# Kernel tuning notes

Hardware: AMD Instinct MI355X
Metric: run time of the kernel (lower is better)

## Reference

```python
import jax, jax.numpy as jnp
import numpy as np

E = 8   # number of experts (= laac_size)
A = 8   # number of agents
B = 2048
S = 256   # per-agent input feature size
H1, H2 = 512, 256          # shallow_dims
D0, D1, D2 = 256, 512, 128  # deep_dims


def setup_inputs() -> dict:
    key = jax.random.key(0)
    ks = jax.random.split(key, 11)
    inputs = jax.random.normal(ks[0], (A, B, S), dtype=jnp.float32)
    laac_shallow = jax.random.randint(ks[1], (1, A), 0, E, dtype=jnp.int64)
    laac_deep = jax.random.randint(ks[2], (1, A), 0, E, dtype=jnp.int64)
    def w(k, shape, fan_in):
        return jax.random.normal(k, shape, dtype=jnp.float32) / np.sqrt(fan_in)
    return {
        "inputs": inputs,
        "laac_shallow": laac_shallow,
        "laac_deep": laac_deep,
        "Ws1": w(ks[3], (E, S, H1), S),  "bs1": jnp.zeros((E, H1), jnp.float32),
        "Ws2": w(ks[4], (E, H1, H2), H1), "bs2": jnp.zeros((E, H2), jnp.float32),
        "Wd1": w(ks[5], (E, D0, D1), D0), "bd1": jnp.zeros((E, D1), jnp.float32),
        "Wd2": w(ks[6], (E, D1, D2), D1), "bd2": jnp.zeros((E, D2), jnp.float32),
    }


def reference(inputs, laac_shallow, laac_deep, Ws1, bs1, Ws2, bs2, Wd1, bd1, Wd2, bd2):
    agent_ids = jnp.arange(A)
    # --- shallow experts: every expert applied to full stacked input [A,B,S] ---
    # Linear -> ReLU -> Linear -> ReLU (final_activation)
    h = jax.nn.relu(jnp.einsum('abi,eih->eabh', inputs, Ws1) + bs1[:, None, None, :])  # [E,A,B,H1]
    sh = jax.nn.relu(jnp.einsum('eabh,eho->eabo', h, Ws2) + bs2[:, None, None, :])     # [E,A,B,H2]
    sel_s = laac_shallow.T[:, 0]             # [A] expert id per agent
    deep_in = sh[sel_s, agent_ids]           # gather over expert dim -> [A,B,H2]
    # --- deep experts: Linear -> ReLU -> Linear (no final activation) ---
    d = jax.nn.relu(jnp.einsum('abi,eih->eabh', deep_in, Wd1) + bd1[:, None, None, :])  # [E,A,B,D1]
    dout = jnp.einsum('eabh,eho->eabo', d, Wd2) + bd2[:, None, None, :]                 # [E,A,B,D2]
    sel_d = laac_deep.T[:, 0]
    out = dout[sel_d, agent_ids]             # [A,B,D2] (original returns this split per agent)
    return out
```

## Files before the change

### kernel.cpp

```cpp
#include <hip/hip_runtime.h>
#include <hip/hip_bf16.h>


typedef __attribute__((ext_vector_type(8))) short bf16x8;
typedef __attribute__((ext_vector_type(4))) float f32x4;

__device__ __forceinline__ ushort f2b(float x) {
    __hip_bfloat16 h = __float2bfloat16(x);
    return *reinterpret_cast<ushort*>(&h);
}

__global__ __launch_bounds__(256)
void prep_weights(const float* __restrict__ Ws1, const float* __restrict__ Ws2,
                  const float* __restrict__ Wd1, const float* __restrict__ Wd2,
                  const int* __restrict__ sel_s, const int* __restrict__ sel_d,
                  ushort* __restrict__ W1p, ushort* __restrict__ W2p,
                  ushort* __restrict__ W3p, ushort* __restrict__ W4p)
{
    const int layer = blockIdx.z;
    const int e  = blockIdx.y;
    const int fg = blockIdx.x;

    const int* sel = (layer <= 1) ? sel_s : sel_d;
    bool used = false;
    #pragma unroll
    for (int a = 0; a < 8; ++a) used |= (sel[a] == e);
    if (!used) return;

    const float* W; ushort* Wp; int K, N;
    if (layer == 0)      { W = Ws1; Wp = W1p; K = 256; N = 512; }
    else if (layer == 1) { W = Ws2; Wp = W2p; K = 512; N = 256; }
    else if (layer == 2) { W = Wd1; Wp = W3p; K = 256; N = 512; }
    else                 { W = Wd2; Wp = W4p; K = 512; N = 128; }
    if (fg >= N / 16) return;
    const int NK = K / 32;
    W += (size_t)e * K * N;

    __shared__ float tile[512][17];
    const int tid = threadIdx.x;
    const int n0 = fg * 16;
    for (int idx = tid; idx < K * 16; idx += 256)
        tile[idx >> 4][idx & 15] = W[(size_t)(idx >> 4) * N + n0 + (idx & 15)];
    __syncthreads();
    ushort* dst = Wp + (((size_t)e * (N / 16) + fg) * NK) * 512;
    for (int w = tid; w < NK * 64; w += 256) {
        const int s    = w >> 6;
        const int lane = w & 63;
        const int c    = lane & 15;
        const int kb   = s * 32 + ((lane >> 4) << 3);
        bf16x8 v;
        #pragma unroll
        for (int j = 0; j < 8; ++j)
            v[j] = (short)f2b(tile[kb + j][c]);
        *reinterpret_cast<bf16x8*>(&dst[(size_t)w * 8]) = v;
    }
}

template<int K, int N, int MG>
__device__ __forceinline__ bf16x8 peekB(const ushort* __restrict__ Wp,
                                        int wid, int lane, int j)
{
    constexpr int NG = 16 / MG;
    constexpr int F  = N / 16 / NG;
    constexpr int NK = K / 32;
    const int wc = wid % NG;
    const ushort* bBase = Wp + ((size_t)(wc * F) * NK) * 512 + (size_t)lane * 8;
    const int f = j % F, s = j / F;
    return *reinterpret_cast<const bf16x8*>(bBase + ((size_t)f * NK + s) * 512);
}

__device__ __forceinline__ bf16x8 peekB4(const ushort* __restrict__ Wp,
                                         int wid, int lane, int j)
{
    const int wc = wid & 7;
    const int kh = wid >> 3;
    return *reinterpret_cast<const bf16x8*>(
        Wp + ((size_t)wc * 16 + kh * 8 + j) * 512 + (size_t)lane * 8);
}

template<int K, int N, int MG, int RELU>
__device__ __forceinline__ void layer_mlp(
    const ushort* __restrict__ Wp, const float* __restrict__ bias,
    const ushort* __restrict__ sIn, ushort* __restrict__ sOut,
    float* __restrict__ gOut, int wid, int lane,
    bf16x8 pb0, bf16x8 pb1)
{
    constexpr int NG = 16 / MG;
    constexpr int F  = N / 16 / NG;
    constexpr int M4 = 4 / MG;
    constexpr int NK = K / 32;
    const int r15 = lane & 15, lh = lane >> 4;
    const int wc = wid % NG, wr = wid / NG;
    const int rowBase = wr * (64 / MG);

    const ushort* bBase = Wp + ((size_t)(wc * F) * NK) * 512 + (size_t)lane * 8;

    float4 bv[F];
    #pragma unroll
    for (int f = 0; f < F; ++f)
        bv[f] = *reinterpret_cast<const float4*>(
            &bias[(wc * F + f) * 16 + lh * 4]);

    f32x4 acc[M4][F];
    #pragma unroll
    for (int m = 0; m < M4; ++m)
        #pragma unroll
        for (int f = 0; f < F; ++f)
            acc[m][f] = (f32x4){0.f, 0.f, 0.f, 0.f};

    #pragma unroll
    for (int s = 0; s < NK; ++s) {
        const int k0 = s * 32;
        bf16x8 a[M4];
        #pragma unroll
        for (int m = 0; m < M4; ++m) {
            const int row  = rowBase + m * 16 + r15;
            const int phys = ((k0 >> 3) + lh) ^ (row & 7);
            a[m] = *reinterpret_cast<const bf16x8*>(
                reinterpret_cast<const char*>(sIn) + row * (K * 2) + (phys << 4));
        }
        bf16x8 b[F];
        #pragma unroll
        for (int f = 0; f < F; ++f) {
            const int j = s * F + f;
            if (j == 0)      b[f] = pb0;
            else if (j == 1) b[f] = pb1;
            else b[f] = *reinterpret_cast<const bf16x8*>(
                     bBase + ((size_t)f * NK + s) * 512);
        }
        #pragma unroll
        for (int m = 0; m < M4; ++m)
            #pragma unroll
            for (int f = 0; f < F; ++f)
                acc[m][f] = __builtin_amdgcn_mfma_f32_16x16x32_bf16(
                    b[f], a[m], acc[m][f], 0, 0, 0);
    }

    #pragma unroll
    for (int f = 0; f < F; ++f) {
        const int cbase = (wc * F + f) * 16 + lh * 4;
        #pragma unroll
        for (int m = 0; m < M4; ++m) {
            const int row = rowBase + m * 16 + r15;
            float v0 = acc[m][f][0] + bv[f].x;
            float v1 = acc[m][f][1] + bv[f].y;
            float v2 = acc[m][f][2] + bv[f].z;
            float v3 = acc[m][f][3] + bv[f].w;
            if (RELU) {
                v0 = fmaxf(v0, 0.f); v1 = fmaxf(v1, 0.f);
                v2 = fmaxf(v2, 0.f); v3 = fmaxf(v3, 0.f);
            }
            if (gOut) {
                *reinterpret_cast<float4*>(&gOut[(size_t)row * N + cbase]) =
                    (float4){v0, v1, v2, v3};
            } else {
                const uint lo = ((uint)f2b(v1) << 16) | (uint)f2b(v0);
                const uint hi = ((uint)f2b(v3) << 16) | (uint)f2b(v2);
                const int byteoff = row * (N * 2) +
                    ((((cbase >> 3) ^ (row & 7))) << 4) + ((cbase & 7) << 1);
                *reinterpret_cast<uint2*>(
                    reinterpret_cast<char*>(sOut) + byteoff) = (uint2){lo, hi};
            }
        }
    }
}

__device__ __forceinline__ int pidx(int row, int col) {
    const int chunk = col >> 2;
    const int phys  = chunk ^ ((row & 7) << 2);
    return row * 128 + (phys << 2);
}

__device__ __forceinline__ void layer_out_ksplit(
    const ushort* __restrict__ Wp, const float* __restrict__ bias,
    const ushort* __restrict__ sIn, float* __restrict__ pLds,
    float* __restrict__ gOut, int wid, int lane,
    bf16x8 pb0, bf16x8 pb1)
{
    constexpr int K = 512, N = 128;
    constexpr int NKH = 8;
    const int r15 = lane & 15, lh = lane >> 4;
    const int wc = wid & 7;
    const int kh = wid >> 3;

    const ushort* bBase = Wp + ((size_t)wc * 16 + kh * 8) * 512 + (size_t)lane * 8;

    const float4 bv = *reinterpret_cast<const float4*>(&bias[wc * 16 + lh * 4]);

    f32x4 acc[4];
    #pragma unroll
    for (int m = 0; m < 4; ++m) acc[m] = (f32x4){0.f, 0.f, 0.f, 0.f};

    #pragma unroll
    for (int s2 = 0; s2 < NKH; ++s2) {
        const int k0 = (kh * NKH + s2) * 32;
        bf16x8 a[4];
        #pragma unroll
        for (int m = 0; m < 4; ++m) {
            const int row  = m * 16 + r15;
            const int phys = ((k0 >> 3) + lh) ^ (row & 7);
            a[m] = *reinterpret_cast<const bf16x8*>(
                reinterpret_cast<const char*>(sIn) + row * (K * 2) + (phys << 4));
        }
        bf16x8 b;
        if (s2 == 0)      b = pb0;
        else if (s2 == 1) b = pb1;
        else b = *reinterpret_cast<const bf16x8*>(bBase + (size_t)s2 * 512);
        #pragma unroll
        for (int m = 0; m < 4; ++m)
            acc[m] = __builtin_amdgcn_mfma_f32_16x16x32_bf16(
                b, a[m], acc[m], 0, 0, 0);
    }

    if (kh == 1) {
        #pragma unroll
        for (int m = 0; m < 4; ++m) {
            const int row = m * 16 + r15;
            const int col = wc * 16 + lh * 4;
            *reinterpret_cast<float4*>(&pLds[pidx(row, col)]) =
                (float4){acc[m][0], acc[m][1], acc[m][2], acc[m][3]};
        }
    }
    __syncthreads();
    if (kh == 0) {
        #pragma unroll
        for (int m = 0; m < 4; ++m) {
            const int row = m * 16 + r15;
            const int col = wc * 16 + lh * 4;
            const float4 p = *reinterpret_cast<const float4*>(&pLds[pidx(row, col)]);
            const float v0 = acc[m][0] + p.x + bv.x;
            const float v1 = acc[m][1] + p.y + bv.y;
            const float v2 = acc[m][2] + p.z + bv.z;
            const float v3 = acc[m][3] + p.w + bv.w;
            *reinterpret_cast<float4*>(&gOut[(size_t)row * N + col]) =
                (float4){v0, v1, v2, v3};
        }
    }
}

__global__ __launch_bounds__(1024, 4)
void madps_fused(const float* __restrict__ X,
                 const int* __restrict__ sel_s, const int* __restrict__ sel_d,
                 const ushort* __restrict__ W1p, const ushort* __restrict__ W2p,
                 const ushort* __restrict__ W3p, const ushort* __restrict__ W4p,
                 const float* __restrict__ bs1, const float* __restrict__ bs2,
                 const float* __restrict__ bd1, const float* __restrict__ bd2,
                 float* __restrict__ out)
{
    constexpr int S = 256, H1 = 512, H2 = 256, D1 = 512, D2 = 128;

    __shared__ __align__(16) ushort buf0[64 * 256];
    __shared__ __align__(16) ushort buf1[64 * 512];

    const int bid   = blockIdx.x;
    const int agent = bid & 7;
    const int rb    = bid >> 3;
    const int tid   = threadIdx.x;
    const int lane  = tid & 63;
    const int wid   = tid >> 6;

    const long long es = sel_s[agent];
    const long long ed = sel_d[agent];

    const ushort* W1e = W1p + (size_t)es * ((H1 / 16) * (S  / 32) * 512);
    const ushort* W2e = W2p + (size_t)es * ((H2 / 16) * (H1 / 32) * 512);
    const ushort* W3e = W3p + (size_t)ed * ((D1 / 16) * (H2 / 32) * 512);
    const ushort* W4e = W4p + (size_t)ed * ((D2 / 16) * (D1 / 32) * 512);

    const float* Xa = X + ((size_t)agent * 2048 + (size_t)rb * 64) * S;

    bf16x8 pb0 = peekB<S, H1, 1>(W1e, wid, lane, 0);
    bf16x8 pb1 = peekB<S, H1, 1>(W1e, wid, lane, 1);

    #pragma unroll
    for (int i = 0; i < 4; ++i) {
        const int flat4 = i * 1024 + tid;
        const int row = flat4 >> 6;
        const int c4  = flat4 & 63;
        const float4 v = reinterpret_cast<const float4*>(Xa)[flat4];
        ushort4 o;
        o.x = f2b(v.x); o.y = f2b(v.y); o.z = f2b(v.z); o.w = f2b(v.w);
        const int byteoff = (((c4 >> 1) ^ (row & 7)) << 4) | ((c4 & 1) << 3);
        *reinterpret_cast<ushort4*>(
            reinterpret_cast<char*>(buf0) + row * 512 + byteoff) = o;
    }
    __syncthreads();

    layer_mlp<S, H1, 1, 1>(W1e, bs1 + es * H1, buf0, buf1, nullptr,
                           wid, lane, pb0, pb1);
    pb0 = peekB<H1, H2, 1>(W2e, wid, lane, 0);
    pb1 = peekB<H1, H2, 1>(W2e, wid, lane, 1);
    __syncthreads();
    layer_mlp<H1, H2, 1, 1>(W2e, bs2 + es * H2, buf1, buf0, nullptr,
                            wid, lane, pb0, pb1);
    pb0 = peekB<H2, D1, 1>(W3e, wid, lane, 0);
    pb1 = peekB<H2, D1, 1>(W3e, wid, lane, 1);
    __syncthreads();
    layer_mlp<H2, D1, 1, 1>(W3e, bd1 + ed * D1, buf0, buf1, nullptr,
                            wid, lane, pb0, pb1);
    pb0 = peekB4(W4e, wid, lane, 0);
    pb1 = peekB4(W4e, wid, lane, 1);
    __syncthreads();
    float* outP = out + ((size_t)agent * 2048 + (size_t)rb * 64) * D2;
    layer_out_ksplit(W4e, bd2 + ed * D2, buf1,
                     reinterpret_cast<float*>(buf0), outP, wid, lane, pb0, pb1);
}

extern "C" void kernel_launch(void* const* d_in, const int* in_sizes, int n_in,
                              void* d_out, int out_size, void* d_ws, size_t ws_size,
                              hipStream_t stream)
{
    constexpr int E = 8, S = 256, H1 = 512, H2 = 256, D1 = 512, D2 = 128;

    const float* inputs = (const float*)d_in[0];
    const int*   sel_s  = (const int*)d_in[1];
    const int*   sel_d  = (const int*)d_in[2];
    const float* Ws1 = (const float*)d_in[3];
    const float* bs1 = (const float*)d_in[4];
    const float* Ws2 = (const float*)d_in[5];
    const float* bs2 = (const float*)d_in[6];
    const float* Wd1 = (const float*)d_in[7];
    const float* bd1 = (const float*)d_in[8];
    const float* Wd2 = (const float*)d_in[9];
    const float* bd2 = (const float*)d_in[10];
    float* out = (float*)d_out;

    ushort* W1p = (ushort*)d_ws;
    ushort* W2p = W1p + (size_t)E * S * H1;
    ushort* W3p = W2p + (size_t)E * H1 * H2;
    ushort* W4p = W3p + (size_t)E * H2 * D1;

    prep_weights<<<dim3(32, E, 4), 256, 0, stream>>>(
        Ws1, Ws2, Wd1, Wd2, sel_s, sel_d, W1p, W2p, W3p, W4p);

    madps_fused<<<dim3(256), dim3(1024), 0, stream>>>(
        inputs, sel_s, sel_d, W1p, W2p, W3p, W4p,
        bs1, bs2, bd1, bd2, out);
}
```

Measured before the change: 32.06 us.

## Move K-split reduction from output layer to second shallow layer

The second shallow layer (512->256) now uses a two-way K-split across the 16 waves, with partial sums reduced through LDS (reusing the input buffer after a barrier) before bias, ReLU and bf16 store. The final 512->128 layer goes back to the generic layer_mlp with MG=2 row groups and no K-split reduction. The intent is to shorten the per-wave dependent MFMA chain on the larger layer and drop the LDS reduction from the small output layer. In exchange, layer 2 gains an extra barrier and an fp32 LDS round trip, and its doubled accumulators raise register pressure.

Measured after the change: 35.24 us. 9.9% more time.

```diff
diff --git a/kernel.cpp b/kernel.cpp
--- a/kernel.cpp
+++ b/kernel.cpp
@@ -69,13 +69,14 @@
     return *reinterpret_cast<const bf16x8*>(bBase + ((size_t)f * NK + s) * 512);
 }
 
-__device__ __forceinline__ bf16x8 peekB4(const ushort* __restrict__ Wp,
-                                         int wid, int lane, int j)
+__device__ __forceinline__ bf16x8 peekB2K(const ushort* __restrict__ Wp,
+                                          int wid, int lane, int j)
 {
     const int wc = wid & 7;
     const int kh = wid >> 3;
+    const int f = j & 1, s2 = j >> 1;
     return *reinterpret_cast<const bf16x8*>(
-        Wp + ((size_t)wc * 16 + kh * 8 + j) * 512 + (size_t)lane * 8);
+        Wp + (((size_t)(wc * 2 + f) * 16) + kh * 8 + s2) * 512 + (size_t)lane * 8);
 }
 
 template<int K, int N, int MG, int RELU>
@@ -165,31 +166,33 @@
     }
 }
 
-__device__ __forceinline__ int pidx(int row, int col) {
+__device__ __forceinline__ int pidx2(int row, int col) {
     const int chunk = col >> 2;
     const int phys  = chunk ^ ((row & 7) << 2);
-    return row * 128 + (phys << 2);
-}
-
-__device__ __forceinline__ void layer_out_ksplit(
+    return row * 256 + (phys << 2);
+}
+
+__device__ __forceinline__ void layer2_ksplit(
     const ushort* __restrict__ Wp, const float* __restrict__ bias,
-    const ushort* __restrict__ sIn, float* __restrict__ pLds,
-    float* __restrict__ gOut, int wid, int lane,
+    ushort* __restrict__ sIn ,
+    ushort* __restrict__ sOut , int wid, int lane,
     bf16x8 pb0, bf16x8 pb1)
 {
-    constexpr int K = 512, N = 128;
+    constexpr int K = 512, N = 256;
     constexpr int NKH = 8;
     const int r15 = lane & 15, lh = lane >> 4;
     const int wc = wid & 7;
     const int kh = wid >> 3;
 
-    const ushort* bBase = Wp + ((size_t)wc * 16 + kh * 8) * 512 + (size_t)lane * 8;
-
-    const float4 bv = *reinterpret_cast<const float4*>(&bias[wc * 16 + lh * 4]);
-
-    f32x4 acc[4];
-    #pragma unroll
-    for (int m = 0; m < 4; ++m) acc[m] = (f32x4){0.f, 0.f, 0.f, 0.f};
+    const float4 bv0 = *reinterpret_cast<const float4*>(&bias[(wc * 2 + 0) * 16 + lh * 4]);
+    const float4 bv1 = *reinterpret_cast<const float4*>(&bias[(wc * 2 + 1) * 16 + lh * 4]);
+
+    f32x4 acc[4][2];
+    #pragma unroll
+    for (int m = 0; m < 4; ++m)
+        #pragma unroll
+        for (int f = 0; f < 2; ++f)
+            acc[m][f] = (f32x4){0.f, 0.f, 0.f, 0.f};
 
     #pragma unroll
     for (int s2 = 0; s2 < NKH; ++s2) {
@@ -202,38 +205,60 @@
             a[m] = *reinterpret_cast<const bf16x8*>(
                 reinterpret_cast<const char*>(sIn) + row * (K * 2) + (phys << 4));
         }
-        bf16x8 b;
-        if (s2 == 0)      b = pb0;
-        else if (s2 == 1) b = pb1;
-        else b = *reinterpret_cast<const bf16x8*>(bBase + (size_t)s2 * 512);
+        bf16x8 b[2];
+        #pragma unroll
+        for (int f = 0; f < 2; ++f) {
+            const int j = s2 * 2 + f;
+            if (j == 0)      b[f] = pb0;
+            else if (j == 1) b[f] = pb1;
+            else b[f] = *reinterpret_cast<const bf16x8*>(
+                     Wp + (((size_t)(wc * 2 + f) * 16) + kh * NKH + s2) * 512
+                        + (size_t)lane * 8);
+        }
         #pragma unroll
         for (int m = 0; m < 4; ++m)
-            acc[m] = __builtin_amdgcn_mfma_f32_16x16x32_bf16(
-                b, a[m], acc[m], 0, 0, 0);
-    }
-
+            #pragma unroll
+            for (int f = 0; f < 2; ++f)
+                acc[m][f] = __builtin_amdgcn_mfma_f32_16x16x32_bf16(
+                    b[f], a[m], acc[m][f], 0, 0, 0);
+    }
+
+    __syncthreads();
+    float* pLds = reinterpret_cast<float*>(sIn);
     if (kh == 1) {
         #pragma unroll
-        for (int m = 0; m < 4; ++m) {
-            const int row = m * 16 + r15;
-            const int col = wc * 16 + lh * 4;
-            *reinterpret_cast<float4*>(&pLds[pidx(row, col)]) =
-                (float4){acc[m][0], acc[m][1], acc[m][2], acc[m][3]};
-        }
+        for (int m = 0; m < 4; ++m)
+            #pragma unroll
+            for (int f = 0; f < 2; ++f) {
+                const int row = m * 16 + r15;
+                const int col = (wc * 2 + f) * 16 + lh * 4;
+                *reinterpret_cast<float4*>(&pLds[pidx2(row, col)]) =
+                    (float4){acc[m][f][0], acc[m][f][1], acc[m][f][2], acc[m][f][3]};
+            }
     }
     __syncthreads();
     if (kh == 0) {
         #pragma unroll
-        for (int m = 0; m < 4; ++m) {
-            const int row = m * 16 + r15;
-            const int col = wc * 16 + lh * 4;
-            const float4 p = *reinterpret_cast<const float4*>(&pLds[pidx(row, col)]);
-            const float v0 = acc[m][0] + p.x + bv.x;
-            const float v1 = acc[m][1] + p.y + bv.y;
-            const float v2 = acc[m][2] + p.z + bv.z;
-            const float v3 = acc[m][3] + p.w + bv.w;
-            *reinterpret_cast<float4*>(&gOut[(size_t)row * N + col]) =
-                (float4){v0, v1, v2, v3};
+        for (int f = 0; f < 2; ++f) {
+            const float4 bv = f ? bv1 : bv0;
+            const int cbase = (wc * 2 + f) * 16 + lh * 4;
+            #pragma unroll
+            for (int m = 0; m < 4; ++m) {
+                const int row = m * 16 + r15;
+                const float4 p = *reinterpret_cast<const float4*>(&pLds[pidx2(row, cbase)]);
+                float v0 = acc[m][f][0] + p.x + bv.x;
+                float v1 = acc[m][f][1] + p.y + bv.y;
+                float v2 = acc[m][f][2] + p.z + bv.z;
+                float v3 = acc[m][f][3] + p.w + bv.w;
+                v0 = fmaxf(v0, 0.f); v1 = fmaxf(v1, 0.f);
+                v2 = fmaxf(v2, 0.f); v3 = fmaxf(v3, 0.f);
+                const uint lo = ((uint)f2b(v1) << 16) | (uint)f2b(v0);
+                const uint hi = ((uint)f2b(v3) << 16) | (uint)f2b(v2);
+                const int byteoff = row * (N * 2) +
+                    ((((cbase >> 3) ^ (row & 7))) << 4) + ((cbase & 7) << 1);
+                *reinterpret_cast<uint2*>(
+                    reinterpret_cast<char*>(sOut) + byteoff) = (uint2){lo, hi};
+            }
         }
     }
 }
@@ -288,22 +313,21 @@
 
     layer_mlp<S, H1, 1, 1>(W1e, bs1 + es * H1, buf0, buf1, nullptr,
                            wid, lane, pb0, pb1);
-    pb0 = peekB<H1, H2, 1>(W2e, wid, lane, 0);
-    pb1 = peekB<H1, H2, 1>(W2e, wid, lane, 1);
-    __syncthreads();
-    layer_mlp<H1, H2, 1, 1>(W2e, bs2 + es * H2, buf1, buf0, nullptr,
-                            wid, lane, pb0, pb1);
+    pb0 = peekB2K(W2e, wid, lane, 0);
+    pb1 = peekB2K(W2e, wid, lane, 1);
+    __syncthreads();
+    layer2_ksplit(W2e, bs2 + es * H2, buf1, buf0, wid, lane, pb0, pb1);
     pb0 = peekB<H2, D1, 1>(W3e, wid, lane, 0);
     pb1 = peekB<H2, D1, 1>(W3e, wid, lane, 1);
     __syncthreads();
     layer_mlp<H2, D1, 1, 1>(W3e, bd1 + ed * D1, buf0, buf1, nullptr,
                             wid, lane, pb0, pb1);
-    pb0 = peekB4(W4e, wid, lane, 0);
-    pb1 = peekB4(W4e, wid, lane, 1);
+    pb0 = peekB<D1, D2, 2>(W4e, wid, lane, 0);
+    pb1 = peekB<D1, D2, 2>(W4e, wid, lane, 1);
     __syncthreads();
     float* outP = out + ((size_t)agent * 2048 + (size_t)rb * 64) * D2;
-    layer_out_ksplit(W4e, bd2 + ed * D2, buf1,
-                     reinterpret_cast<float*>(buf0), outP, wid, lane, pb0, pb1);
+    layer_mlp<D1, D2, 2, 0>(W4e, bd2 + ed * D2, buf1, nullptr, outP,
+                            wid, lane, pb0, pb1);
 }
 
 extern "C" void kernel_launch(void* const* d_in, const int* in_sizes, int n_in,
```
